# Performance work log

Measured on AMD Instinct MI355X. Metric: run time of the kernel, lower is better.

The kernel has to match this reference:

```python
import jax, jax.numpy as jnp
import numpy as np

B, S, W, D, H = 2, 2048, 32, 1024, 16

def setup_inputs() -> dict:
    key = jax.random.key(0)
    ks = jax.random.split(key, 8)
    scale = 0.02
    return {
        'q': jax.random.normal(ks[0], (B, S, D), jnp.float32),
        'k': jax.random.normal(ks[1], (B, S, W, D), jnp.float32),
        'v': jax.random.normal(ks[2], (B, S, W, D), jnp.float32),
        'Wq': jax.random.normal(ks[3], (D, D), jnp.float32) * scale,
        'bq': jnp.zeros((D,), jnp.float32),
        'Wk': jax.random.normal(ks[4], (D, D), jnp.float32) * scale,
        'bk': jnp.zeros((D,), jnp.float32),
        'Wv': jax.random.normal(ks[5], (D, D), jnp.float32) * scale,
        'bv': jnp.zeros((D,), jnp.float32),
        'Wo': jax.random.normal(ks[6], (D, D), jnp.float32) * scale,
        'bo': jnp.zeros((D,), jnp.float32),
        'num_heads': H,
    }

def reference(q, k, v, Wq, bq, Wk, bk, Wv, bv, Wo, bo, num_heads):
    b, s, d = q.shape
    w = k.shape[2]
    hd = d // num_heads
    # query: Linear -> view(B,S,H,1,hd) -> transpose(1,2) => (B,H,S,1,hd)
    qh = (q @ Wq.T + bq).reshape(b, s, num_heads, 1, hd).transpose(0, 2, 1, 3, 4)
    # key/value: Linear then RAW view (B,H,S,W,hd) -- faithful to torch .view (no head transpose)
    kh = (k @ Wk.T + bk).reshape(b, num_heads, s, w, hd)
    vh = (v @ Wv.T + bv).reshape(b, num_heads, s, w, hd)
    # scores: (B,H,S,1,W), scaled by sqrt(head_dim) (query.shape[-1] inside attention)
    scores = jnp.einsum('bhsid,bhswd->bhsiw', qh, kh) / jnp.sqrt(jnp.float32(hd))
    # Softmax(dim=1) normalizes over the HEAD axis -- faithful to the original
    attn = jax.nn.softmax(scores, axis=1)
    A = jnp.einsum('bhsiw,bhswd->bhsid', attn, vh)[:, :, :, 0, :]  # (B,H,S,hd)
    out = A.reshape(b, s, d)  # raw view, matches torch .view(B,S,D)
    return out @ Wo.T + bo
```

## Files before the change

kernel.cpp:

```cpp
#include <hip/hip_runtime.h>
#include <hip/hip_bf16.h>


#define DEVI __device__ __forceinline__

typedef __attribute__((ext_vector_type(8))) short bf16x8;
typedef __attribute__((ext_vector_type(4))) float f32x4;
typedef const __attribute__((address_space(1))) void* gvp;
typedef __attribute__((address_space(3))) void* lvp;

DEVI ushort f2bf(float f) {
  uint u = __float_as_uint(f);
  u = u + 0x7fffu + ((u >> 16) & 1u);
  return (ushort)(u >> 16);
}
DEVI float bf2f(ushort u) { return __uint_as_float(((uint)u) << 16); }

__global__ __launch_bounds__(256) void cast_kernel(const float* __restrict__ in,
                                                   ushort* __restrict__ out,
                                                   long n) {
  long i = ((long)blockIdx.x * 256 + threadIdx.x) * 8;
  const long stride = (long)gridDim.x * 256 * 8;
  for (; i < n; i += stride) {
    float4 a = *reinterpret_cast<const float4*>(in + i);
    float4 b = *reinterpret_cast<const float4*>(in + i + 4);
    ushort o[8];
    o[0] = f2bf(a.x); o[1] = f2bf(a.y); o[2] = f2bf(a.z); o[3] = f2bf(a.w);
    o[4] = f2bf(b.x); o[5] = f2bf(b.y); o[6] = f2bf(b.z); o[7] = f2bf(b.w);
    *reinterpret_cast<int4*>(out + i) = *reinterpret_cast<const int4*>(o);
  }
}

__global__ __launch_bounds__(512, 2) void gemm_big(const ushort* __restrict__ Ag,
                                                   const ushort* __restrict__ Wg,
                                                   const float* __restrict__ bias,
                                                   ushort* __restrict__ Cg) {
  constexpr int K = 1024;
  constexpr int NT = 32;
  constexpr int SLOT = 32768;
  __shared__ char lds[4 * SLOT];
  const int tid = threadIdx.x;
  const int lane = tid & 63;
  const int wave = tid >> 6;
  const int wm = wave >> 2;
  const int wn = wave & 3;
  const int d = blockIdx.x;
  const int bn = (d >> 3) & 3;
  const size_t bm = (size_t)(d & 7) * (gridDim.x >> 5) + (d >> 5);

  const ushort* aB = Ag + bm * 256 * K;
  const ushort* bB = Wg + (size_t)bn * 256 * K;

  const int ar0 = tid >> 2, ac0 = (tid & 3) ^ ((ar0 >> 1) & 3);
  const int ar1 = (tid + 512) >> 2, ac1 = (tid & 3) ^ ((ar1 >> 1) & 3);
  const ushort* aS0 = aB + (size_t)ar0 * K + ac0 * 8;
  const ushort* aS1 = aB + (size_t)ar1 * K + ac1 * 8;
  const ushort* bS0 = bB + (size_t)ar0 * K + ac0 * 8;
  const ushort* bS1 = bB + (size_t)ar1 * K + ac1 * 8;
  const int adst0 = tid * 16;
  const int adst1 = tid * 16 + 8192;
  const int bdst0 = 16384 + tid * 16;
  const int bdst1 = 24576 + tid * 16;

  const int lm = lane & 15;
  const int cs = (lm >> 1) & 3;
  const int cSwz = ((lane >> 4) ^ cs) * 16;
  const int offA = lm * 64 + cSwz + wm * 8192;
  const int offB = 16384 + lm * 64 + cSwz + wn * 4096;

  f32x4 acc[8][4] = {};

#define STAGE_T(slotOff, ktElem)                                                   \
  {                                                                                \
    __builtin_amdgcn_global_load_lds((gvp)(aS0 + (ktElem)),                        \
                                     (lvp)(lds + (slotOff) + adst0), 16, 0, 0);    \
    __builtin_amdgcn_global_load_lds((gvp)(aS1 + (ktElem)),                        \
                                     (lvp)(lds + (slotOff) + adst1), 16, 0, 0);    \
    __builtin_amdgcn_global_load_lds((gvp)(bS0 + (ktElem)),                        \
                                     (lvp)(lds + (slotOff) + bdst0), 16, 0, 0);    \
    __builtin_amdgcn_global_load_lds((gvp)(bS1 + (ktElem)),                        \
                                     (lvp)(lds + (slotOff) + bdst1), 16, 0, 0);    \
  }

  STAGE_T(0 * SLOT, 0);
  STAGE_T(1 * SLOT, 32);
  STAGE_T(2 * SLOT, 64);
  __builtin_amdgcn_sched_barrier(0);
  asm volatile("s_waitcnt vmcnt(8)" ::: "memory");
  __builtin_amdgcn_s_barrier();
  __builtin_amdgcn_sched_barrier(0);

  int rdOff = 0, stOff = 3 * SLOT;
  for (int t = 0; t < NT; ++t) {
    if (t + 3 < NT) STAGE_T(stOff, (t + 3) * 32);
    const char* pA = lds + rdOff + offA;
    const char* pB = lds + rdOff + offB;
    bf16x8 a[8], b[4];
#pragma unroll
    for (int fi = 0; fi < 8; ++fi)
      a[fi] = *reinterpret_cast<const bf16x8*>(pA + fi * 1024);
#pragma unroll
    for (int fj = 0; fj < 4; ++fj)
      b[fj] = *reinterpret_cast<const bf16x8*>(pB + fj * 1024);
    __builtin_amdgcn_s_setprio(1);
#pragma unroll
    for (int fi = 0; fi < 8; ++fi)
#pragma unroll
      for (int fj = 0; fj < 4; ++fj)
        acc[fi][fj] = __builtin_amdgcn_mfma_f32_16x16x32_bf16(a[fi], b[fj],
                                                              acc[fi][fj], 0, 0, 0);
    __builtin_amdgcn_s_setprio(0);
    if (t < NT - 1) {
      __builtin_amdgcn_sched_barrier(0);
      if (t <= NT - 4)
        asm volatile("s_waitcnt vmcnt(8)" ::: "memory");
      else if (t == NT - 3)
        asm volatile("s_waitcnt vmcnt(4)" ::: "memory");
      else
        asm volatile("s_waitcnt vmcnt(0)" ::: "memory");
      __builtin_amdgcn_s_barrier();
      __builtin_amdgcn_sched_barrier(0);
    }
    rdOff = (rdOff == 3 * SLOT) ? 0 : rdOff + SLOT;
    stOff = (stOff == 3 * SLOT) ? 0 : stOff + SLOT;
  }
#undef STAGE_T

#pragma unroll
  for (int fi = 0; fi < 8; ++fi) {
#pragma unroll
    for (int fj = 0; fj < 4; ++fj) {
      int n = bn * 256 + wn * 64 + fj * 16 + lm;
      float bv = bias[n];
#pragma unroll
      for (int r = 0; r < 4; ++r) {
        size_t m = bm * 256 + wm * 128 + fi * 16 + ((lane >> 4) * 4) + r;
        Cg[m * 1024 + n] = f2bf(acc[fi][fj][r] + bv);
      }
    }
  }
}

template <typename TOUT>
__global__ __launch_bounds__(256) void gemm_lds(const ushort* __restrict__ Ag,
                                                const ushort* __restrict__ Wg,
                                                const float* __restrict__ bias,
                                                TOUT* __restrict__ Cg) {
  constexpr int K = 1024;
  __shared__ ushort lA[128 * 64];
  __shared__ ushort lB[128 * 64];
  const int tid = threadIdx.x;
  const int lane = tid & 63;
  const int wave = tid >> 6;
  const int wr = (wave >> 1) * 64;
  const int wc = (wave & 1) * 64;
  const int d = blockIdx.x;
  const int bn = (d >> 3) & 7;
  const size_t bm = (size_t)(d & 7) * (gridDim.x >> 6) + (d >> 6);

  const ushort* aB = Ag + bm * 128 * K;
  const ushort* bB = Wg + (size_t)bn * 128 * K;
  const int srow = wave * 32 + (lane >> 3);
  const int scol = ((lane & 7) ^ (lane >> 3)) * 8;
  char* lAc = (char*)lA;
  char* lBc = (char*)lB;

  f32x4 acc[4][4] = {};

  for (int kt = 0; kt < K; kt += 64) {
    __syncthreads();
#pragma unroll
    for (int c = 0; c < 4; ++c) {
      __builtin_amdgcn_global_load_lds(
          (gvp)(aB + (size_t)(srow + c * 8) * K + kt + scol),
          (lvp)(lAc + wave * 4096 + c * 1024), 16, 0, 0);
      __builtin_amdgcn_global_load_lds(
          (gvp)(bB + (size_t)(srow + c * 8) * K + kt + scol),
          (lvp)(lBc + wave * 4096 + c * 1024), 16, 0, 0);
    }
    __syncthreads();
#pragma unroll
    for (int kk = 0; kk < 2; ++kk) {
      bf16x8 af[4], bg[4];
#pragma unroll
      for (int fi = 0; fi < 4; ++fi) {
        int r = wr + fi * 16 + (lane & 15);
        int byte = (r * 128 + kk * 64 + ((lane >> 4) * 16)) ^ ((r & 7) << 4);
        af[fi] = *reinterpret_cast<const bf16x8*>(lAc + byte);
      }
#pragma unroll
      for (int fj = 0; fj < 4; ++fj) {
        int r = wc + fj * 16 + (lane & 15);
        int byte = (r * 128 + kk * 64 + ((lane >> 4) * 16)) ^ ((r & 7) << 4);
        bg[fj] = *reinterpret_cast<const bf16x8*>(lBc + byte);
      }
#pragma unroll
      for (int fi = 0; fi < 4; ++fi)
#pragma unroll
        for (int fj = 0; fj < 4; ++fj)
          acc[fi][fj] = __builtin_amdgcn_mfma_f32_16x16x32_bf16(af[fi], bg[fj],
                                                                acc[fi][fj], 0, 0, 0);
    }
  }
#pragma unroll
  for (int fi = 0; fi < 4; ++fi) {
#pragma unroll
    for (int fj = 0; fj < 4; ++fj) {
      int n = bn * 128 + wc + fj * 16 + (lane & 15);
      float bv = bias[n];
#pragma unroll
      for (int r = 0; r < 4; ++r) {
        size_t m = bm * 128 + wr + fi * 16 + ((lane >> 4) * 4) + r;
        float val = acc[fi][fj][r] + bv;
        if constexpr (sizeof(TOUT) == 2)
          reinterpret_cast<ushort*>(Cg)[m * 1024 + n] = f2bf(val);
        else
          reinterpret_cast<float*>(Cg)[m * 1024 + n] = val;
      }
    }
  }
}

template <typename TIN, typename TOUT>
__global__ __launch_bounds__(256) void gemm_bias(const TIN* __restrict__ Ag,
                                                 const float* __restrict__ Wg,
                                                 const float* __restrict__ bias,
                                                 TOUT* __restrict__ Cg) {
  constexpr int K = 1024;
  __shared__ char lA[128 * 64 * 2];
  __shared__ char lB[128 * 64 * 2];
  const int tid = threadIdx.x;
  const int lane = tid & 63;
  const int wave = tid >> 6;
  const int wr = (wave >> 1) * 64;
  const int wc = (wave & 1) * 64;
  const int bn = blockIdx.x;
  const size_t bm = blockIdx.y;

  const TIN* aBase = Ag + bm * 128 * K;
  const float* bBase = Wg + (size_t)bn * 128 * K;

  f32x4 acc[4][4] = {};

  for (int kt = 0; kt < K; kt += 64) {
    __syncthreads();
    if constexpr (sizeof(TIN) == 4) {
#pragma unroll
      for (int i = 0; i < 8; ++i) {
        int f = tid + i * 256;
        int row = f >> 4, c4 = f & 15;
        const float4 v = *reinterpret_cast<const float4*>(
            reinterpret_cast<const float*>(aBase) + (size_t)row * K + kt + c4 * 4);
        ushort4 pk;
        pk.x = f2bf(v.x); pk.y = f2bf(v.y); pk.z = f2bf(v.z); pk.w = f2bf(v.w);
        int byte = (row * 128 + c4 * 8) ^ ((row & 7) << 4);
        *reinterpret_cast<ushort4*>(lA + byte) = pk;
      }
    } else {
#pragma unroll
      for (int i = 0; i < 4; ++i) {
        int f = tid + i * 256;
        int row = f >> 3, c8 = f & 7;
        int4 v = *reinterpret_cast<const int4*>(
            reinterpret_cast<const ushort*>(aBase) + (size_t)row * K + kt + c8 * 8);
        int byte = (row * 128 + c8 * 16) ^ ((row & 7) << 4);
        *reinterpret_cast<int4*>(lA + byte) = v;
      }
    }
#pragma unroll
    for (int i = 0; i < 8; ++i) {
      int f = tid + i * 256;
      int row = f >> 4, c4 = f & 15;
      const float4 v =
          *reinterpret_cast<const float4*>(bBase + (size_t)row * K + kt + c4 * 4);
      ushort4 pk;
      pk.x = f2bf(v.x); pk.y = f2bf(v.y); pk.z = f2bf(v.z); pk.w = f2bf(v.w);
      int byte = (row * 128 + c4 * 8) ^ ((row & 7) << 4);
      *reinterpret_cast<ushort4*>(lB + byte) = pk;
    }
    __syncthreads();
#pragma unroll
    for (int kk = 0; kk < 2; ++kk) {
      bf16x8 af[4], bg[4];
#pragma unroll
      for (int fi = 0; fi < 4; ++fi) {
        int r = wr + fi * 16 + (lane & 15);
        int byte = (r * 128 + kk * 64 + ((lane >> 4) * 16)) ^ ((r & 7) << 4);
        af[fi] = *reinterpret_cast<const bf16x8*>(lA + byte);
      }
#pragma unroll
      for (int fj = 0; fj < 4; ++fj) {
        int r = wc + fj * 16 + (lane & 15);
        int byte = (r * 128 + kk * 64 + ((lane >> 4) * 16)) ^ ((r & 7) << 4);
        bg[fj] = *reinterpret_cast<const bf16x8*>(lB + byte);
      }
#pragma unroll
      for (int fi = 0; fi < 4; ++fi)
#pragma unroll
        for (int fj = 0; fj < 4; ++fj)
          acc[fi][fj] =
              __builtin_amdgcn_mfma_f32_16x16x32_bf16(af[fi], bg[fj], acc[fi][fj], 0, 0, 0);
    }
  }
#pragma unroll
  for (int fi = 0; fi < 4; ++fi) {
#pragma unroll
    for (int fj = 0; fj < 4; ++fj) {
      int n = bn * 128 + wc + fj * 16 + (lane & 15);
      float bv = bias[n];
#pragma unroll
      for (int r = 0; r < 4; ++r) {
        size_t m = bm * 128 + wr + fi * 16 + ((lane >> 4) * 4) + r;
        float val = acc[fi][fj][r] + bv;
        if constexpr (sizeof(TOUT) == 2)
          reinterpret_cast<ushort*>(Cg)[m * 1024 + n] = f2bf(val);
        else
          reinterpret_cast<float*>(Cg)[m * 1024 + n] = val;
      }
    }
  }
}

__global__ __launch_bounds__(512) void attn_kernel(const ushort* __restrict__ Q,
                                                   const ushort* __restrict__ Kl,
                                                   const ushort* __restrict__ Vl,
                                                   ushort* __restrict__ Aout) {
  const int bs = blockIdx.x;
  const int b = bs >> 11, sp = bs & 2047;
  const int tid = threadIdx.x;
  const int wave = tid >> 6, lane = tid & 63;

  __shared__ ushort qrow[1024];
  __shared__ float sc[16][32];
  __shared__ float attnw[16][32];
  __shared__ float mx[32], rinv[32];

  reinterpret_cast<uint*>(qrow)[tid] =
      reinterpret_cast<const uint*>(Q + (size_t)bs * 1024)[tid];
  __syncthreads();

  const int wp = lane & 31, half = lane >> 5;
#pragma unroll
  for (int hh = 0; hh < 2; ++hh) {
    const int h = wave * 2 + hh;
    const int s_k = h * 128 + (sp >> 4);
    const int w_k = (sp & 15) * 2 + (wp >> 4);
    const ushort* kp =
        Kl + (((size_t)(b * 2048 + s_k) * 32) + w_k) * 1024 + (wp & 15) * 64 + half * 32;
    const ushort* qp = qrow + h * 64 + half * 32;
    float dot = 0.f;
#pragma unroll
    for (int j = 0; j < 32; j += 8) {
      int4 kv = *reinterpret_cast<const int4*>(kp + j);
      int4 qv = *reinterpret_cast<const int4*>(qp + j);
      const ushort* ka = reinterpret_cast<const ushort*>(&kv);
      const ushort* qa = reinterpret_cast<const ushort*>(&qv);
#pragma unroll
      for (int t = 0; t < 8; ++t) dot += bf2f(ka[t]) * bf2f(qa[t]);
    }
    dot += __shfl_xor(dot, 32);
    if (half == 0) sc[h][wp] = dot * 0.125f;
  }
  __syncthreads();
  if (tid < 32) {
    float m = sc[0][tid];
#pragma unroll
    for (int h = 1; h < 16; ++h) m = fmaxf(m, sc[h][tid]);
    float s = 0.f;
#pragma unroll
    for (int h = 0; h < 16; ++h) s += __expf(sc[h][tid] - m);
    mx[tid] = m;
    rinv[tid] = 1.f / s;
  }
  __syncthreads();
  if (lane < 32) {
#pragma unroll
    for (int hh = 0; hh < 2; ++hh) {
      const int h = wave * 2 + hh;
      attnw[h][lane] = __expf(sc[h][lane] - mx[lane]) * rinv[lane];
    }
  }
  __syncthreads();
#pragma unroll
  for (int hh = 0; hh < 2; ++hh) {
    const int h = wave * 2 + hh;
    const int s_k = h * 128 + (sp >> 4);
    const size_t vb = (((size_t)(b * 2048 + s_k) * 32) + (sp & 15) * 2) * 1024;
    float a = 0.f;
#pragma unroll
    for (int w2 = 0; w2 < 32; ++w2) {
      float wgt = attnw[h][w2];
      a += wgt * bf2f(Vl[vb + (size_t)(w2 >> 4) * 1024 + (w2 & 15) * 64 + lane]);
    }
    Aout[(((size_t)(b * 16 + h)) * 2048 + sp) * 64 + lane] = f2bf(a);
  }
}

extern "C" void kernel_launch(void* const* d_in, const int* in_sizes, int n_in,
                              void* d_out, int out_size, void* d_ws, size_t ws_size,
                              hipStream_t stream) {
  const float* q = (const float*)d_in[0];
  const float* k = (const float*)d_in[1];
  const float* v = (const float*)d_in[2];
  const float* Wq = (const float*)d_in[3];
  const float* bq = (const float*)d_in[4];
  const float* Wk = (const float*)d_in[5];
  const float* bk = (const float*)d_in[6];
  const float* Wv = (const float*)d_in[7];
  const float* bv = (const float*)d_in[8];
  const float* Wo = (const float*)d_in[9];
  const float* bo = (const float*)d_in[10];
  float* out = (float*)d_out;

  char* ws = (char*)d_ws;
  const size_t MB = 1u << 20;
  ushort* Qlin = (ushort*)ws;
  ushort* Aws  = (ushort*)(ws + 8 * MB);
  ushort* wkbf = (ushort*)(ws + 16 * MB);
  ushort* wvbf = (ushort*)(ws + 18 * MB);
  ushort* wqbf = (ushort*)(ws + 20 * MB);
  ushort* wobf = (ushort*)(ws + 22 * MB);
  ushort* qbf  = (ushort*)(ws + 24 * MB);
  ushort* Klin = (ushort*)(ws + 32 * MB);
  ushort* Vlin = (ushort*)(ws + 288 * MB);
  ushort* kvbf = (ushort*)(ws + 544 * MB);
  const bool full = ws_size >= 800 * MB;

  const long NKV = 134217728L;

  if (full) {
    cast_kernel<<<dim3(512), 256, 0, stream>>>(Wq, wqbf, 1048576L);
    cast_kernel<<<dim3(512), 256, 0, stream>>>(Wk, wkbf, 1048576L);
    cast_kernel<<<dim3(512), 256, 0, stream>>>(Wv, wvbf, 1048576L);
    cast_kernel<<<dim3(512), 256, 0, stream>>>(Wo, wobf, 1048576L);
    cast_kernel<<<dim3(2048), 256, 0, stream>>>(q, qbf, 4194304L);
    gemm_lds<ushort><<<dim3(256), 256, 0, stream>>>(qbf, wqbf, bq, Qlin);
    cast_kernel<<<dim3(4096), 256, 0, stream>>>(k, kvbf, NKV);
    gemm_big<<<dim3(2048), 512, 0, stream>>>(kvbf, wkbf, bk, Klin);
    cast_kernel<<<dim3(4096), 256, 0, stream>>>(v, kvbf, NKV);
    gemm_big<<<dim3(2048), 512, 0, stream>>>(kvbf, wvbf, bv, Vlin);
    attn_kernel<<<dim3(4096), dim3(512), 0, stream>>>(Qlin, Klin, Vlin, Aws);
    gemm_lds<float><<<dim3(256), 256, 0, stream>>>(Aws, wobf, bo, out);
  } else {
    gemm_bias<float, ushort><<<dim3(8, 32), 256, 0, stream>>>(q, Wq, bq, Qlin);
    gemm_bias<float, ushort><<<dim3(8, 1024), 256, 0, stream>>>(k, Wk, bk, Klin);
    gemm_bias<float, ushort><<<dim3(8, 1024), 256, 0, stream>>>(v, Wv, bv, Vlin);
    attn_kernel<<<dim3(4096), dim3(512), 0, stream>>>(Qlin, Klin, Vlin, Aws);
    gemm_bias<ushort, float><<<dim3(8, 32), 256, 0, stream>>>(Aws, Wo, bo, out);
  }
}
```

Baseline: 1.072 ms.

## Restructure big GEMM main loop into 8-phase ping-pong with BK=64 tiles

Replaces the 4-slot BK=32 ring buffer in the big projection GEMM with two 64-wide K buffers. Each K-tile is split into four quadrant phases, and global-to-LDS loads for upcoming tiles are interleaved between the MFMA blocks under barriers, ping-pong style. The LDS swizzle changes to an 8-chunk XOR pattern for 128-byte rows. The goal is finer overlap of memory traffic, LDS reads and MFMA work, at the cost of many more barriers and more complex vmcnt bookkeeping.

```diff
diff --git a/kernel.cpp b/kernel.cpp
--- a/kernel.cpp
+++ b/kernel.cpp
@@ -31,14 +31,27 @@
   }
 }
 
+template <int FI0, int FJ0>
+DEVI void mfma16(f32x4 (&acc)[8][4], const bf16x8 (&A)[4][2],
+                 const bf16x8 (&B)[2][2]) {
+  __builtin_amdgcn_s_setprio(1);
+#pragma unroll
+  for (int i = 0; i < 4; ++i)
+#pragma unroll
+    for (int j = 0; j < 2; ++j)
+#pragma unroll
+      for (int kk = 0; kk < 2; ++kk)
+        acc[FI0 + i][FJ0 + j] = __builtin_amdgcn_mfma_f32_16x16x32_bf16(
+            A[i][kk], B[j][kk], acc[FI0 + i][FJ0 + j], 0, 0, 0);
+  __builtin_amdgcn_s_setprio(0);
+}
+
 __global__ __launch_bounds__(512, 2) void gemm_big(const ushort* __restrict__ Ag,
                                                    const ushort* __restrict__ Wg,
                                                    const float* __restrict__ bias,
                                                    ushort* __restrict__ Cg) {
   constexpr int K = 1024;
-  constexpr int NT = 32;
-  constexpr int SLOT = 32768;
-  __shared__ char lds[4 * SLOT];
+  __shared__ char lds[131072];
   const int tid = threadIdx.x;
   const int lane = tid & 63;
   const int wave = tid >> 6;
@@ -51,80 +64,135 @@
   const ushort* aB = Ag + bm * 256 * K;
   const ushort* bB = Wg + (size_t)bn * 256 * K;
 
-  const int ar0 = tid >> 2, ac0 = (tid & 3) ^ ((ar0 >> 1) & 3);
-  const int ar1 = (tid + 512) >> 2, ac1 = (tid & 3) ^ ((ar1 >> 1) & 3);
-  const ushort* aS0 = aB + (size_t)ar0 * K + ac0 * 8;
-  const ushort* aS1 = aB + (size_t)ar1 * K + ac1 * 8;
-  const ushort* bS0 = bB + (size_t)ar0 * K + ac0 * 8;
-  const ushort* bS1 = bB + (size_t)ar1 * K + ac1 * 8;
-  const int adst0 = tid * 16;
-  const int adst1 = tid * 16 + 8192;
-  const int bdst0 = 16384 + tid * 16;
-  const int bdst1 = 24576 + tid * 16;
+  const int r0 = tid >> 3;
+  const int c0 = (tid & 7) ^ (r0 & 7);
+  const ushort* aS0 = aB + (size_t)r0 * K + c0 * 8;
+  const ushort* aS1 = aB + (size_t)(r0 + 64) * K + c0 * 8;
+  const ushort* aS2 = aB + (size_t)(r0 + 128) * K + c0 * 8;
+  const ushort* aS3 = aB + (size_t)(r0 + 192) * K + c0 * 8;
+  const ushort* bS0 = bB + (size_t)r0 * K + c0 * 8;
+  const ushort* bS1 = bB + (size_t)(r0 + 64) * K + c0 * 8;
+  const ushort* bS2 = bB + (size_t)(r0 + 128) * K + c0 * 8;
+  const ushort* bS3 = bB + (size_t)(r0 + 192) * K + c0 * 8;
+  const int dst0 = tid * 16;
+  const int dst1 = tid * 16 + 8192;
 
   const int lm = lane & 15;
-  const int cs = (lm >> 1) & 3;
-  const int cSwz = ((lane >> 4) ^ cs) * 16;
-  const int offA = lm * 64 + cSwz + wm * 8192;
-  const int offB = 16384 + lm * 64 + cSwz + wn * 4096;
+  const int q = lane >> 4;
+  const int rowB = lm * 128;
+  const int swz0 = (q ^ (lm & 7)) * 16;
+  const int swz1 = ((4 + q) ^ (lm & 7)) * 16;
+  const char* ldsc = (const char*)lds;
+  const char* p0A = ldsc + wm * 16384 + rowB;
+  const char* p0B = ldsc + 32768 + (wn >> 1) * 16384 + (wn & 1) * 8192 + rowB;
+  const char* p1A = p0A + 65536;
+  const char* p1B = p0B + 65536;
 
   f32x4 acc[8][4] = {};
-
-#define STAGE_T(slotOff, ktElem)                                                   \
-  {                                                                                \
-    __builtin_amdgcn_global_load_lds((gvp)(aS0 + (ktElem)),                        \
-                                     (lvp)(lds + (slotOff) + adst0), 16, 0, 0);    \
-    __builtin_amdgcn_global_load_lds((gvp)(aS1 + (ktElem)),                        \
-                                     (lvp)(lds + (slotOff) + adst1), 16, 0, 0);    \
-    __builtin_amdgcn_global_load_lds((gvp)(bS0 + (ktElem)),                        \
-                                     (lvp)(lds + (slotOff) + bdst0), 16, 0, 0);    \
-    __builtin_amdgcn_global_load_lds((gvp)(bS1 + (ktElem)),                        \
-                                     (lvp)(lds + (slotOff) + bdst1), 16, 0, 0);    \
-  }
-
-  STAGE_T(0 * SLOT, 0);
-  STAGE_T(1 * SLOT, 32);
-  STAGE_T(2 * SLOT, 64);
+  bf16x8 aF[4][2], aG[4][2], bF[2][2], bG[2][2];
+
+#define STG(p0, p1, kb, ldsOff)                                                  \
+  {                                                                              \
+    __builtin_amdgcn_global_load_lds((gvp)((p0) + (kb)),                         \
+                                     (lvp)(lds + (ldsOff) + dst0), 16, 0, 0);    \
+    __builtin_amdgcn_global_load_lds((gvp)((p1) + (kb)),                         \
+                                     (lvp)(lds + (ldsOff) + dst1), 16, 0, 0);    \
+  }
+#define PH_SYNC()                                    \
+  __builtin_amdgcn_s_barrier();                      \
+  asm volatile("s_waitcnt lgkmcnt(0)" ::: "memory"); \
   __builtin_amdgcn_sched_barrier(0);
-  asm volatile("s_waitcnt vmcnt(8)" ::: "memory");
+#define LDA(dst, p)                                                          \
+  _Pragma("unroll") for (int i_ = 0; i_ < 4; ++i_) {                         \
+    dst[i_][0] = *reinterpret_cast<const bf16x8*>((p) + i_ * 2048 + swz0);   \
+    dst[i_][1] = *reinterpret_cast<const bf16x8*>((p) + i_ * 2048 + swz1);   \
+  }
+#define LDB(dst, p)                                                          \
+  _Pragma("unroll") for (int j_ = 0; j_ < 2; ++j_) {                         \
+    dst[j_][0] = *reinterpret_cast<const bf16x8*>((p) + j_ * 2048 + swz0);   \
+    dst[j_][1] = *reinterpret_cast<const bf16x8*>((p) + j_ * 2048 + swz1);   \
+  }
+
+  STG(aS0, aS1, 0, 0);
+  STG(aS2, aS3, 0, 16384);
+  STG(bS0, bS1, 0, 32768);
+  STG(bS2, bS3, 0, 49152);
+  STG(aS0, aS1, 64, 65536);
+  STG(aS2, aS3, 64, 65536 + 16384);
+  __builtin_amdgcn_sched_barrier(0);
+  asm volatile("s_waitcnt vmcnt(4)" ::: "memory");
   __builtin_amdgcn_s_barrier();
   __builtin_amdgcn_sched_barrier(0);
 
-  int rdOff = 0, stOff = 3 * SLOT;
-  for (int t = 0; t < NT; ++t) {
-    if (t + 3 < NT) STAGE_T(stOff, (t + 3) * 32);
-    const char* pA = lds + rdOff + offA;
-    const char* pB = lds + rdOff + offB;
-    bf16x8 a[8], b[4];
-#pragma unroll
-    for (int fi = 0; fi < 8; ++fi)
-      a[fi] = *reinterpret_cast<const bf16x8*>(pA + fi * 1024);
-#pragma unroll
-    for (int fj = 0; fj < 4; ++fj)
-      b[fj] = *reinterpret_cast<const bf16x8*>(pB + fj * 1024);
-    __builtin_amdgcn_s_setprio(1);
-#pragma unroll
-    for (int fi = 0; fi < 8; ++fi)
-#pragma unroll
-      for (int fj = 0; fj < 4; ++fj)
-        acc[fi][fj] = __builtin_amdgcn_mfma_f32_16x16x32_bf16(a[fi], b[fj],
-                                                              acc[fi][fj], 0, 0, 0);
-    __builtin_amdgcn_s_setprio(0);
-    if (t < NT - 1) {
+  for (int it = 0; it < 8; ++it) {
+    const int kb1 = it * 128 + 64;
+    const int kb2 = it * 128 + 128;
+    const int kb3 = it * 128 + 192;
+    const bool pf = (it < 7);
+
+    LDA(aF, p0A);
+    LDB(bF, p0B);
+    STG(bS0, bS1, kb1, 65536 + 32768);
+    PH_SYNC();
+    mfma16<0, 0>(acc, aF, bF);
+    __builtin_amdgcn_s_barrier();
+
+    LDA(aG, p0A + 8192);
+    STG(bS2, bS3, kb1, 65536 + 49152);
+    PH_SYNC();
+    mfma16<4, 0>(acc, aG, bF);
+    __builtin_amdgcn_s_barrier();
+
+    LDB(bG, p0B + 4096);
+    if (pf) STG(aS0, aS1, kb2, 0);
+    PH_SYNC();
+    mfma16<0, 2>(acc, aF, bG);
+    __builtin_amdgcn_s_barrier();
+
+    if (pf) STG(aS2, aS3, kb2, 16384);
+    PH_SYNC();
+    mfma16<4, 2>(acc, aG, bG);
+    __builtin_amdgcn_sched_barrier(0);
+    if (pf)
+      asm volatile("s_waitcnt vmcnt(4)" ::: "memory");
+    else
+      asm volatile("s_waitcnt vmcnt(0)" ::: "memory");
+    __builtin_amdgcn_s_barrier();
+    __builtin_amdgcn_sched_barrier(0);
+
+    LDA(aF, p1A);
+    LDB(bF, p1B);
+    if (pf) STG(bS0, bS1, kb2, 32768);
+    PH_SYNC();
+    mfma16<0, 0>(acc, aF, bF);
+    __builtin_amdgcn_s_barrier();
+
+    LDA(aG, p1A + 8192);
+    if (pf) STG(bS2, bS3, kb2, 49152);
+    PH_SYNC();
+    mfma16<4, 0>(acc, aG, bF);
+    __builtin_amdgcn_s_barrier();
+
+    LDB(bG, p1B + 4096);
+    if (pf) STG(aS0, aS1, kb3, 65536);
+    PH_SYNC();
+    mfma16<0, 2>(acc, aF, bG);
+    __builtin_amdgcn_s_barrier();
+
+    if (pf) STG(aS2, aS3, kb3, 65536 + 16384);
+    PH_SYNC();
+    mfma16<4, 2>(acc, aG, bG);
+    if (it < 7) {
       __builtin_amdgcn_sched_barrier(0);
-      if (t <= NT - 4)
-        asm volatile("s_waitcnt vmcnt(8)" ::: "memory");
-      else if (t == NT - 3)
-        asm volatile("s_waitcnt vmcnt(4)" ::: "memory");
-      else
-        asm volatile("s_waitcnt vmcnt(0)" ::: "memory");
+      asm volatile("s_waitcnt vmcnt(4)" ::: "memory");
       __builtin_amdgcn_s_barrier();
       __builtin_amdgcn_sched_barrier(0);
     }
-    rdOff = (rdOff == 3 * SLOT) ? 0 : rdOff + SLOT;
-    stOff = (stOff == 3 * SLOT) ? 0 : stOff + SLOT;
-  }
-#undef STAGE_T
+  }
+#undef STG
+#undef PH_SYNC
+#undef LDA
+#undef LDB
 
 #pragma unroll
   for (int fi = 0; fi < 8; ++fi) {
```

After: 1.049 ms. -2.2%, faster.

## Fuse fp32-to-bf16 cast of K/V into the big projection GEMM loader

Applied to the files above, without the earlier changes.

The projection GEMM now reads fp32 K and V directly, converts them to bf16 in registers with packed convert instructions, and writes them to LDS. This replaces the separate cast kernels and the bf16 staging buffer. The intent is to remove a full extra read/write pass over the two largest tensors. The cost is register-staged A loads instead of async global-to-LDS loads, a software-pipelined prefetch one stage ahead, and a full barrier every iteration, which may reduce GEMM efficiency.

```diff
diff --git a/kernel.cpp b/kernel.cpp
--- a/kernel.cpp
+++ b/kernel.cpp
@@ -31,10 +31,10 @@
   }
 }
 
-__global__ __launch_bounds__(512, 2) void gemm_big(const ushort* __restrict__ Ag,
-                                                   const ushort* __restrict__ Wg,
-                                                   const float* __restrict__ bias,
-                                                   ushort* __restrict__ Cg) {
+__global__ __launch_bounds__(512)
+__attribute__((amdgpu_waves_per_eu(2, 2)))
+void gemm_big(const float* __restrict__ Ag, const ushort* __restrict__ Wg,
+              const float* __restrict__ bias, ushort* __restrict__ Cg) {
   constexpr int K = 1024;
   constexpr int NT = 32;
   constexpr int SLOT = 32768;
@@ -48,15 +48,14 @@
   const int bn = (d >> 3) & 3;
   const size_t bm = (size_t)(d & 7) * (gridDim.x >> 5) + (d >> 5);
 
-  const ushort* aB = Ag + bm * 256 * K;
   const ushort* bB = Wg + (size_t)bn * 256 * K;
 
-  const int ar0 = tid >> 2, ac0 = (tid & 3) ^ ((ar0 >> 1) & 3);
-  const int ar1 = (tid + 512) >> 2, ac1 = (tid & 3) ^ ((ar1 >> 1) & 3);
-  const ushort* aS0 = aB + (size_t)ar0 * K + ac0 * 8;
-  const ushort* aS1 = aB + (size_t)ar1 * K + ac1 * 8;
+  const int ar0 = tid >> 2;
+  const int ac0 = (tid & 3) ^ ((ar0 >> 1) & 3);
+  const float* pA0 = Ag + bm * 256 * K + (size_t)ar0 * K + ac0 * 8;
+  const float* pA1 = pA0 + (size_t)128 * K;
   const ushort* bS0 = bB + (size_t)ar0 * K + ac0 * 8;
-  const ushort* bS1 = bB + (size_t)ar1 * K + ac1 * 8;
+  const ushort* bS1 = bB + (size_t)(ar0 + 128) * K + ac0 * 8;
   const int adst0 = tid * 16;
   const int adst1 = tid * 16 + 8192;
   const int bdst0 = 16384 + tid * 16;
@@ -67,34 +66,60 @@
   const int cSwz = ((lane >> 4) ^ cs) * 16;
   const int offA = lm * 64 + cSwz + wm * 8192;
   const int offB = 16384 + lm * 64 + cSwz + wn * 4096;
+  const char* ldsc = (const char*)lds;
 
   f32x4 acc[8][4] = {};
-
-#define STAGE_T(slotOff, ktElem)                                                   \
-  {                                                                                \
-    __builtin_amdgcn_global_load_lds((gvp)(aS0 + (ktElem)),                        \
-                                     (lvp)(lds + (slotOff) + adst0), 16, 0, 0);    \
-    __builtin_amdgcn_global_load_lds((gvp)(aS1 + (ktElem)),                        \
-                                     (lvp)(lds + (slotOff) + adst1), 16, 0, 0);    \
-    __builtin_amdgcn_global_load_lds((gvp)(bS0 + (ktElem)),                        \
-                                     (lvp)(lds + (slotOff) + bdst0), 16, 0, 0);    \
-    __builtin_amdgcn_global_load_lds((gvp)(bS1 + (ktElem)),                        \
-                                     (lvp)(lds + (slotOff) + bdst1), 16, 0, 0);    \
-  }
-
-  STAGE_T(0 * SLOT, 0);
-  STAGE_T(1 * SLOT, 32);
-  STAGE_T(2 * SLOT, 64);
-  __builtin_amdgcn_sched_barrier(0);
-  asm volatile("s_waitcnt vmcnt(8)" ::: "memory");
+  float4 st[4];
+
+#define SB0 __builtin_amdgcn_sched_barrier(0)
+#define AISS4(ktE)                                               \
+  {                                                              \
+    st[0] = *reinterpret_cast<const float4*>(pA0 + (ktE));       \
+    st[1] = *reinterpret_cast<const float4*>(pA0 + (ktE) + 4);   \
+    st[2] = *reinterpret_cast<const float4*>(pA1 + (ktE));       \
+    st[3] = *reinterpret_cast<const float4*>(pA1 + (ktE) + 4);   \
+  }
+#define CVT4(base)                                                           \
+  {                                                                          \
+    uint w0, w1, w2, w3;                                                     \
+    asm("v_cvt_pk_bf16_f32 %0,%1,%2" : "=v"(w0) : "v"(st[0].x), "v"(st[0].y)); \
+    asm("v_cvt_pk_bf16_f32 %0,%1,%2" : "=v"(w1) : "v"(st[0].z), "v"(st[0].w)); \
+    asm("v_cvt_pk_bf16_f32 %0,%1,%2" : "=v"(w2) : "v"(st[1].x), "v"(st[1].y)); \
+    asm("v_cvt_pk_bf16_f32 %0,%1,%2" : "=v"(w3) : "v"(st[1].z), "v"(st[1].w)); \
+    *reinterpret_cast<uint4*>(lds + (base) + adst0) = make_uint4(w0, w1, w2, w3); \
+    asm("v_cvt_pk_bf16_f32 %0,%1,%2" : "=v"(w0) : "v"(st[2].x), "v"(st[2].y)); \
+    asm("v_cvt_pk_bf16_f32 %0,%1,%2" : "=v"(w1) : "v"(st[2].z), "v"(st[2].w)); \
+    asm("v_cvt_pk_bf16_f32 %0,%1,%2" : "=v"(w2) : "v"(st[3].x), "v"(st[3].y)); \
+    asm("v_cvt_pk_bf16_f32 %0,%1,%2" : "=v"(w3) : "v"(st[3].z), "v"(st[3].w)); \
+    *reinterpret_cast<uint4*>(lds + (base) + adst1) = make_uint4(w0, w1, w2, w3); \
+  }
+#define STGB(ktE, base)                                                        \
+  {                                                                            \
+    __builtin_amdgcn_global_load_lds((gvp)(bS0 + (ktE)),                       \
+                                     (lvp)(lds + (base) + bdst0), 16, 0, 0);   \
+    __builtin_amdgcn_global_load_lds((gvp)(bS1 + (ktE)),                       \
+                                     (lvp)(lds + (base) + bdst1), 16, 0, 0);   \
+  }
+
+  AISS4(0);  SB0; CVT4(0 * SLOT); SB0;
+  AISS4(32); SB0; CVT4(1 * SLOT); SB0;
+  AISS4(64); SB0; CVT4(2 * SLOT); SB0;
+  STGB(0, 0 * SLOT);
+  STGB(32, 1 * SLOT);
+  STGB(64, 2 * SLOT);
+  AISS4(96); SB0;
+  asm volatile("s_waitcnt vmcnt(0)" ::: "memory");
+  asm volatile("s_waitcnt lgkmcnt(0)" ::: "memory");
   __builtin_amdgcn_s_barrier();
-  __builtin_amdgcn_sched_barrier(0);
+  SB0;
 
   int rdOff = 0, stOff = 3 * SLOT;
   for (int t = 0; t < NT; ++t) {
-    if (t + 3 < NT) STAGE_T(stOff, (t + 3) * 32);
-    const char* pA = lds + rdOff + offA;
-    const char* pB = lds + rdOff + offB;
+    if (t + 3 < NT) CVT4(stOff);
+    if (t + 4 < NT) AISS4((t + 4) * 32);
+    if (t + 3 < NT) STGB((t + 3) * 32, stOff);
+    const char* pA = ldsc + rdOff + offA;
+    const char* pB = ldsc + rdOff + offB;
     bf16x8 a[8], b[4];
 #pragma unroll
     for (int fi = 0; fi < 8; ++fi)
@@ -110,21 +135,18 @@
         acc[fi][fj] = __builtin_amdgcn_mfma_f32_16x16x32_bf16(a[fi], b[fj],
                                                               acc[fi][fj], 0, 0, 0);
     __builtin_amdgcn_s_setprio(0);
-    if (t < NT - 1) {
-      __builtin_amdgcn_sched_barrier(0);
-      if (t <= NT - 4)
-        asm volatile("s_waitcnt vmcnt(8)" ::: "memory");
-      else if (t == NT - 3)
-        asm volatile("s_waitcnt vmcnt(4)" ::: "memory");
-      else
-        asm volatile("s_waitcnt vmcnt(0)" ::: "memory");
-      __builtin_amdgcn_s_barrier();
-      __builtin_amdgcn_sched_barrier(0);
-    }
+    if (t >= NT - 3 && t < NT - 1) {
+      SB0;
+      asm volatile("s_waitcnt vmcnt(0)" ::: "memory");
+    }
+    __builtin_amdgcn_s_barrier();
     rdOff = (rdOff == 3 * SLOT) ? 0 : rdOff + SLOT;
     stOff = (stOff == 3 * SLOT) ? 0 : stOff + SLOT;
   }
-#undef STAGE_T
+#undef AISS4
+#undef CVT4
+#undef STGB
+#undef SB0
 
 #pragma unroll
   for (int fi = 0; fi < 8; ++fi) {
@@ -423,10 +445,7 @@
   ushort* qbf  = (ushort*)(ws + 24 * MB);
   ushort* Klin = (ushort*)(ws + 32 * MB);
   ushort* Vlin = (ushort*)(ws + 288 * MB);
-  ushort* kvbf = (ushort*)(ws + 544 * MB);
   const bool full = ws_size >= 800 * MB;
-
-  const long NKV = 134217728L;
 
   if (full) {
     cast_kernel<<<dim3(512), 256, 0, stream>>>(Wq, wqbf, 1048576L);
@@ -435,10 +454,8 @@
     cast_kernel<<<dim3(512), 256, 0, stream>>>(Wo, wobf, 1048576L);
     cast_kernel<<<dim3(2048), 256, 0, stream>>>(q, qbf, 4194304L);
     gemm_lds<ushort><<<dim3(256), 256, 0, stream>>>(qbf, wqbf, bq, Qlin);
-    cast_kernel<<<dim3(4096), 256, 0, stream>>>(k, kvbf, NKV);
-    gemm_big<<<dim3(2048), 512, 0, stream>>>(kvbf, wkbf, bk, Klin);
-    cast_kernel<<<dim3(4096), 256, 0, stream>>>(v, kvbf, NKV);
-    gemm_big<<<dim3(2048), 512, 0, stream>>>(kvbf, wvbf, bv, Vlin);
+    gemm_big<<<dim3(2048), 512, 0, stream>>>(k, wkbf, bk, Klin);
+    gemm_big<<<dim3(2048), 512, 0, stream>>>(v, wvbf, bv, Vlin);
     attn_kernel<<<dim3(4096), dim3(512), 0, stream>>>(Qlin, Klin, Vlin, Aws);
     gemm_lds<float><<<dim3(256), 256, 0, stream>>>(Aws, wobf, bo, out);
   } else {
```

Result: faster. 928.2 us (-13.4%).

## Fuse fp32-to-bf16 cast of K/V into a single combined K/V projection GEMM

Applied to the files above, without the earlier changes.

Replaces the separate cast kernels and the large pipelined GEMM for the K and V projections with one GEMM launch that reads fp32 K/V directly, converts to bf16 in registers and writes them into swizzled LDS. This removes the write and re-read of the 256MB bf16 intermediate buffers per tensor. It also merges the four weight casts into one launch. The cost is a simpler, unpipelined 128x128 tile GEMM with a single LDS buffer and fp32 loads in the inner loop, which may lower MFMA utilisation compared with the old multi-stage design.

```diff
diff --git a/kernel.cpp b/kernel.cpp
--- a/kernel.cpp
+++ b/kernel.cpp
@@ -31,110 +31,116 @@
   }
 }
 
-__global__ __launch_bounds__(512, 2) void gemm_big(const ushort* __restrict__ Ag,
-                                                   const ushort* __restrict__ Wg,
-                                                   const float* __restrict__ bias,
-                                                   ushort* __restrict__ Cg) {
+__global__ __launch_bounds__(256) void cast4_kernel(const float* __restrict__ i0,
+                                                    const float* __restrict__ i1,
+                                                    const float* __restrict__ i2,
+                                                    const float* __restrict__ i3,
+                                                    ushort* __restrict__ o0,
+                                                    ushort* __restrict__ o1,
+                                                    ushort* __restrict__ o2,
+                                                    ushort* __restrict__ o3) {
+  const long n = 1048576L;
+  long i = ((long)blockIdx.x * 256 + threadIdx.x) * 8;
+  const long stride = (long)gridDim.x * 256 * 8;
+  for (; i < n; i += stride) {
+#pragma unroll
+    for (int m = 0; m < 4; ++m) {
+      const float* in = (m == 0) ? i0 : (m == 1) ? i1 : (m == 2) ? i2 : i3;
+      ushort* out = (m == 0) ? o0 : (m == 1) ? o1 : (m == 2) ? o2 : o3;
+      float4 a = *reinterpret_cast<const float4*>(in + i);
+      float4 b = *reinterpret_cast<const float4*>(in + i + 4);
+      ushort o[8];
+      o[0] = f2bf(a.x); o[1] = f2bf(a.y); o[2] = f2bf(a.z); o[3] = f2bf(a.w);
+      o[4] = f2bf(b.x); o[5] = f2bf(b.y); o[6] = f2bf(b.z); o[7] = f2bf(b.w);
+      *reinterpret_cast<int4*>(out + i) = *reinterpret_cast<const int4*>(o);
+    }
+  }
+}
+
+__global__ __launch_bounds__(256)
+void gemm_mid(const float* __restrict__ A0, const ushort* __restrict__ W0,
+              const float* __restrict__ b0, ushort* __restrict__ C0,
+              const float* __restrict__ A1, const ushort* __restrict__ W1,
+              const float* __restrict__ b1, ushort* __restrict__ C1) {
   constexpr int K = 1024;
-  constexpr int NT = 32;
-  constexpr int SLOT = 32768;
-  __shared__ char lds[4 * SLOT];
+  __shared__ ushort lA[128 * 64];
+  __shared__ ushort lB[128 * 64];
   const int tid = threadIdx.x;
   const int lane = tid & 63;
   const int wave = tid >> 6;
-  const int wm = wave >> 2;
-  const int wn = wave & 3;
-  const int d = blockIdx.x;
-  const int bn = (d >> 3) & 3;
-  const size_t bm = (size_t)(d & 7) * (gridDim.x >> 5) + (d >> 5);
-
-  const ushort* aB = Ag + bm * 256 * K;
-  const ushort* bB = Wg + (size_t)bn * 256 * K;
-
-  const int ar0 = tid >> 2, ac0 = (tid & 3) ^ ((ar0 >> 1) & 3);
-  const int ar1 = (tid + 512) >> 2, ac1 = (tid & 3) ^ ((ar1 >> 1) & 3);
-  const ushort* aS0 = aB + (size_t)ar0 * K + ac0 * 8;
-  const ushort* aS1 = aB + (size_t)ar1 * K + ac1 * 8;
-  const ushort* bS0 = bB + (size_t)ar0 * K + ac0 * 8;
-  const ushort* bS1 = bB + (size_t)ar1 * K + ac1 * 8;
-  const int adst0 = tid * 16;
-  const int adst1 = tid * 16 + 8192;
-  const int bdst0 = 16384 + tid * 16;
-  const int bdst1 = 24576 + tid * 16;
-
-  const int lm = lane & 15;
-  const int cs = (lm >> 1) & 3;
-  const int cSwz = ((lane >> 4) ^ cs) * 16;
-  const int offA = lm * 64 + cSwz + wm * 8192;
-  const int offB = 16384 + lm * 64 + cSwz + wn * 4096;
-
-  f32x4 acc[8][4] = {};
-
-#define STAGE_T(slotOff, ktElem)                                                   \
-  {                                                                                \
-    __builtin_amdgcn_global_load_lds((gvp)(aS0 + (ktElem)),                        \
-                                     (lvp)(lds + (slotOff) + adst0), 16, 0, 0);    \
-    __builtin_amdgcn_global_load_lds((gvp)(aS1 + (ktElem)),                        \
-                                     (lvp)(lds + (slotOff) + adst1), 16, 0, 0);    \
-    __builtin_amdgcn_global_load_lds((gvp)(bS0 + (ktElem)),                        \
-                                     (lvp)(lds + (slotOff) + bdst0), 16, 0, 0);    \
-    __builtin_amdgcn_global_load_lds((gvp)(bS1 + (ktElem)),                        \
-                                     (lvp)(lds + (slotOff) + bdst1), 16, 0, 0);    \
-  }
-
-  STAGE_T(0 * SLOT, 0);
-  STAGE_T(1 * SLOT, 32);
-  STAGE_T(2 * SLOT, 64);
-  __builtin_amdgcn_sched_barrier(0);
-  asm volatile("s_waitcnt vmcnt(8)" ::: "memory");
-  __builtin_amdgcn_s_barrier();
-  __builtin_amdgcn_sched_barrier(0);
-
-  int rdOff = 0, stOff = 3 * SLOT;
-  for (int t = 0; t < NT; ++t) {
-    if (t + 3 < NT) STAGE_T(stOff, (t + 3) * 32);
-    const char* pA = lds + rdOff + offA;
-    const char* pB = lds + rdOff + offB;
-    bf16x8 a[8], b[4];
-#pragma unroll
-    for (int fi = 0; fi < 8; ++fi)
-      a[fi] = *reinterpret_cast<const bf16x8*>(pA + fi * 1024);
-#pragma unroll
-    for (int fj = 0; fj < 4; ++fj)
-      b[fj] = *reinterpret_cast<const bf16x8*>(pB + fj * 1024);
-    __builtin_amdgcn_s_setprio(1);
-#pragma unroll
-    for (int fi = 0; fi < 8; ++fi)
-#pragma unroll
-      for (int fj = 0; fj < 4; ++fj)
-        acc[fi][fj] = __builtin_amdgcn_mfma_f32_16x16x32_bf16(a[fi], b[fj],
-                                                              acc[fi][fj], 0, 0, 0);
-    __builtin_amdgcn_s_setprio(0);
-    if (t < NT - 1) {
-      __builtin_amdgcn_sched_barrier(0);
-      if (t <= NT - 4)
-        asm volatile("s_waitcnt vmcnt(8)" ::: "memory");
-      else if (t == NT - 3)
-        asm volatile("s_waitcnt vmcnt(4)" ::: "memory");
-      else
-        asm volatile("s_waitcnt vmcnt(0)" ::: "memory");
-      __builtin_amdgcn_s_barrier();
-      __builtin_amdgcn_sched_barrier(0);
-    }
-    rdOff = (rdOff == 3 * SLOT) ? 0 : rdOff + SLOT;
-    stOff = (stOff == 3 * SLOT) ? 0 : stOff + SLOT;
-  }
-#undef STAGE_T
-
-#pragma unroll
-  for (int fi = 0; fi < 8; ++fi) {
+  const int wr = (wave >> 1) * 64;
+  const int wc = (wave & 1) * 64;
+  const int half_sel = blockIdx.x >> 13;
+  const int d = blockIdx.x & 8191;
+  const float* Ag = half_sel ? A1 : A0;
+  const ushort* Wg = half_sel ? W1 : W0;
+  const float* bias = half_sel ? b1 : b0;
+  ushort* Cg = half_sel ? C1 : C0;
+  const int bn = (d >> 3) & 7;
+  const size_t bm = (size_t)(d & 7) * 128 + (d >> 6);
+
+  const float* aB = Ag + bm * 128 * K;
+  const ushort* bB = Wg + (size_t)bn * 128 * K;
+  const int srow = wave * 32 + (lane >> 3);
+  const int scol = ((lane & 7) ^ (lane >> 3)) * 8;
+  char* lAc = (char*)lA;
+  char* lBc = (char*)lB;
+
+  f32x4 acc[4][4] = {};
+
+  for (int kt = 0; kt < K; kt += 64) {
+    __syncthreads();
+#pragma unroll
+    for (int c = 0; c < 4; ++c) {
+      __builtin_amdgcn_global_load_lds(
+          (gvp)(bB + (size_t)(srow + c * 8) * K + kt + scol),
+          (lvp)(lBc + wave * 4096 + c * 1024), 16, 0, 0);
+    }
+#pragma unroll
+    for (int i = 0; i < 8; ++i) {
+      int f = tid + i * 256;
+      int row = f >> 4, c4 = f & 15;
+      const float4 v = *reinterpret_cast<const float4*>(
+          aB + (size_t)row * K + kt + c4 * 4);
+      uint w0, w1;
+      asm("v_cvt_pk_bf16_f32 %0,%1,%2" : "=v"(w0) : "v"(v.x), "v"(v.y));
+      asm("v_cvt_pk_bf16_f32 %0,%1,%2" : "=v"(w1) : "v"(v.z), "v"(v.w));
+      int byte = (row * 128 + c4 * 8) ^ ((row & 7) << 4);
+      *reinterpret_cast<uint2*>(lAc + byte) = make_uint2(w0, w1);
+    }
+    __syncthreads();
+#pragma unroll
+    for (int kk = 0; kk < 2; ++kk) {
+      bf16x8 af[4], bg[4];
+#pragma unroll
+      for (int fi = 0; fi < 4; ++fi) {
+        int r = wr + fi * 16 + (lane & 15);
+        int byte = (r * 128 + kk * 64 + ((lane >> 4) * 16)) ^ ((r & 7) << 4);
+        af[fi] = *reinterpret_cast<const bf16x8*>(lAc + byte);
+      }
+#pragma unroll
+      for (int fj = 0; fj < 4; ++fj) {
+        int r = wc + fj * 16 + (lane & 15);
+        int byte = (r * 128 + kk * 64 + ((lane >> 4) * 16)) ^ ((r & 7) << 4);
+        bg[fj] = *reinterpret_cast<const bf16x8*>(lBc + byte);
+      }
+#pragma unroll
+      for (int fi = 0; fi < 4; ++fi)
+#pragma unroll
+        for (int fj = 0; fj < 4; ++fj)
+          acc[fi][fj] = __builtin_amdgcn_mfma_f32_16x16x32_bf16(af[fi], bg[fj],
+                                                                acc[fi][fj], 0, 0, 0);
+    }
+  }
+#pragma unroll
+  for (int fi = 0; fi < 4; ++fi) {
 #pragma unroll
     for (int fj = 0; fj < 4; ++fj) {
-      int n = bn * 256 + wn * 64 + fj * 16 + lm;
+      int n = bn * 128 + wc + fj * 16 + (lane & 15);
       float bv = bias[n];
 #pragma unroll
       for (int r = 0; r < 4; ++r) {
-        size_t m = bm * 256 + wm * 128 + fi * 16 + ((lane >> 4) * 4) + r;
+        size_t m = bm * 128 + wr + fi * 16 + ((lane >> 4) * 4) + r;
         Cg[m * 1024 + n] = f2bf(acc[fi][fj][r] + bv);
       }
     }
@@ -423,22 +429,15 @@
   ushort* qbf  = (ushort*)(ws + 24 * MB);
   ushort* Klin = (ushort*)(ws + 32 * MB);
   ushort* Vlin = (ushort*)(ws + 288 * MB);
-  ushort* kvbf = (ushort*)(ws + 544 * MB);
   const bool full = ws_size >= 800 * MB;
 
-  const long NKV = 134217728L;
-
   if (full) {
-    cast_kernel<<<dim3(512), 256, 0, stream>>>(Wq, wqbf, 1048576L);
-    cast_kernel<<<dim3(512), 256, 0, stream>>>(Wk, wkbf, 1048576L);
-    cast_kernel<<<dim3(512), 256, 0, stream>>>(Wv, wvbf, 1048576L);
-    cast_kernel<<<dim3(512), 256, 0, stream>>>(Wo, wobf, 1048576L);
+    cast4_kernel<<<dim3(512), 256, 0, stream>>>(Wq, Wk, Wv, Wo,
+                                                wqbf, wkbf, wvbf, wobf);
     cast_kernel<<<dim3(2048), 256, 0, stream>>>(q, qbf, 4194304L);
     gemm_lds<ushort><<<dim3(256), 256, 0, stream>>>(qbf, wqbf, bq, Qlin);
-    cast_kernel<<<dim3(4096), 256, 0, stream>>>(k, kvbf, NKV);
-    gemm_big<<<dim3(2048), 512, 0, stream>>>(kvbf, wkbf, bk, Klin);
-    cast_kernel<<<dim3(4096), 256, 0, stream>>>(v, kvbf, NKV);
-    gemm_big<<<dim3(2048), 512, 0, stream>>>(kvbf, wvbf, bv, Vlin);
+    gemm_mid<<<dim3(16384), 256, 0, stream>>>(k, wkbf, bk, Klin,
+                                              v, wvbf, bv, Vlin);
     attn_kernel<<<dim3(4096), dim3(512), 0, stream>>>(Qlin, Klin, Vlin, Aws);
     gemm_lds<float><<<dim3(256), 256, 0, stream>>>(Aws, wobf, bo, out);
   } else {
```

Measured after the change: 1.256 ms. +17.1%, slower.
